# Kernel tuning notes

Measured on AMD Instinct MI355X. Metric: run time of the kernel, lower is better.

Reference implementation:

```python
import jax, jax.numpy as jnp
import numpy as np

N_NODES = 100000
N_EDGES = 3200000
NUM_GRAPHS = 128
IN_DIM = 15
HID = 64


def setup_inputs() -> dict:
    key = jax.random.key(0)
    ks = jax.random.split(key, 12)
    x = jax.random.normal(ks[0], (N_NODES, IN_DIM), dtype=jnp.float32)
    edge_index = jax.random.randint(ks[1], (2, N_EDGES), 0, N_NODES, dtype=jnp.int64)
    batch = jnp.sort(jax.random.randint(ks[2], (N_NODES,), 0, NUM_GRAPHS, dtype=jnp.int64))
    # Glorot-style weights for the 4 GCNConv layers, zero biases (PyG default)
    def glorot(k, fan_in, fan_out):
        s = jnp.sqrt(6.0 / (fan_in + fan_out))
        return jax.random.uniform(k, (fan_in, fan_out), jnp.float32, -s, s)
    return {
        "x": x,
        "w1": glorot(ks[3], IN_DIM, HID), "b1": jnp.zeros((HID,), jnp.float32),
        "w2": glorot(ks[4], HID, HID),    "b2": jnp.zeros((HID,), jnp.float32),
        "w3": glorot(ks[5], HID, HID),    "b3": jnp.zeros((HID,), jnp.float32),
        "w4": glorot(ks[6], HID, HID),    "b4": jnp.zeros((HID,), jnp.float32),
        "edge_index": edge_index,
        "batch": batch,
    }


def _gcn_norm(edge_index, num_nodes):
    # PyG gcn_norm with add_self_loops=True: A_hat = A + I, norm = d^-1/2[src] * d^-1/2[dst]
    loops = jnp.arange(num_nodes, dtype=edge_index.dtype)
    src = jnp.concatenate([edge_index[0], loops])
    dst = jnp.concatenate([edge_index[1], loops])
    deg = jax.ops.segment_sum(jnp.ones_like(dst, dtype=jnp.float32), dst,
                              num_segments=num_nodes)
    dis = jnp.where(deg > 0, jax.lax.rsqrt(deg), 0.0)
    norm = dis[src] * dis[dst]  # [E + N]
    return src, dst, norm


def _gcn_conv(h, w, b, src, dst, norm, num_nodes):
    h = h @ w                               # linear transform first (PyG order)
    msg = h[src] * norm[:, None]            # gather + scale  [E+N, HID]
    agg = jax.ops.segment_sum(msg, dst, num_segments=num_nodes)  # scatter-add
    return agg + b


def reference(x, w1, b1, w2, b2, w3, b3, w4, b4, edge_index, batch):
    n = x.shape[0]
    src, dst, norm = _gcn_norm(edge_index, n)
    h = jax.nn.relu(_gcn_conv(x, w1, b1, src, dst, norm, n))
    h = jax.nn.relu(_gcn_conv(h, w2, b2, src, dst, norm, n))
    h = jax.nn.relu(_gcn_conv(h, w3, b3, src, dst, norm, n))
    h = jax.nn.relu(_gcn_conv(h, w4, b4, src, dst, norm, n))
    # global_mean_pool over graph ids
    sums = jax.ops.segment_sum(h, batch, num_segments=NUM_GRAPHS)
    cnts = jax.ops.segment_sum(jnp.ones((n,), jnp.float32), batch,
                               num_segments=NUM_GRAPHS)
    return sums / jnp.maximum(cnts, 1.0)[:, None]
```

## Files before the change

kernel.cpp:

```cpp
#include <hip/hip_runtime.h>
#include <hip/hip_fp16.h>

#define NN 100000
#define NE 3200000
#define NG 128
#define HID 64

#define BSH 9
#define BNODES 512
#define NBK ((NN + BNODES - 1) / BNODES)
#define CCH 4096

typedef __attribute__((ext_vector_type(2))) _Float16 half2v;
typedef __attribute__((ext_vector_type(4))) _Float16 half4v;

#if __has_builtin(__builtin_amdgcn_fdot2)
#define FDOT2(v, o, a) __builtin_amdgcn_fdot2((v), (o), (a), false)
#else
static __device__ inline float FDOT2(half2v v, half2v o, float a) {
    return a + (float)v.x * (float)o.x + (float)v.y * (float)o.y;
}
#endif

__global__ __launch_bounds__(256) void bcount_kernel(const int* __restrict__ dst,
                                                     int* __restrict__ bcnt, int E) {
    __shared__ int h[NBK];
    for (int i = threadIdx.x; i < NBK; i += 256) h[i] = 0;
    __syncthreads();
    for (int e = blockIdx.x * 256 + threadIdx.x; e < E; e += gridDim.x * 256)
        atomicAdd(&h[dst[e] >> BSH], 1);
    __syncthreads();
    for (int i = threadIdx.x; i < NBK; i += 256)
        if (h[i]) atomicAdd(&bcnt[i], h[i]);
}

__global__ __launch_bounds__(256) void bscan_kernel(const int* __restrict__ bcnt,
                                                    int* __restrict__ bbase,
                                                    int* __restrict__ bcur, int E) {
    __shared__ int s[NBK];
    int t = threadIdx.x;
    if (t < NBK) s[t] = bcnt[t];
    __syncthreads();
    if (t == 0) {
        int acc = 0;
        for (int i = 0; i < NBK; ++i) { int v = s[i]; s[i] = acc; acc += v; }
    }
    __syncthreads();
    if (t < NBK) { bbase[t] = s[t]; bcur[t] = s[t]; }
    if (t == 0) bbase[NBK] = E;
}

__global__ __launch_bounds__(256) void bscatter_kernel(const int* __restrict__ src,
                                                       const int* __restrict__ dst,
                                                       int* __restrict__ bcur,
                                                       unsigned* __restrict__ pairs,
                                                       int E) {
    __shared__ unsigned stage[CCH];
    __shared__ unsigned char bb[CCH];
    __shared__ int cnt[NBK];
    __shared__ int base[NBK];
    const int e0 = blockIdx.x * CCH;
    const int n  = min(CCH, E - e0);
    if (n <= 0) return;
    for (int i = threadIdx.x; i < NBK; i += 256) cnt[i] = 0;
    __syncthreads();
    for (int i = threadIdx.x; i < n; i += 256) {
        int s = src[e0 + i], d = dst[e0 + i];
        int b = d >> BSH;
        stage[i] = ((unsigned)(d & (BNODES - 1)) << 17) | (unsigned)s;
        bb[i] = (unsigned char)b;
        atomicAdd(&cnt[b], 1);
    }
    __syncthreads();
    for (int i = threadIdx.x; i < NBK; i += 256) {
        int c = cnt[i];
        base[i] = c ? atomicAdd(&bcur[i], c) : 0;
        cnt[i] = 0;
    }
    __syncthreads();
    for (int i = threadIdx.x; i < n; i += 256) {
        int b = bb[i];
        int pos = base[b] + atomicAdd(&cnt[b], 1);
        pairs[pos] = stage[i];
    }
}

__global__ __launch_bounds__(256) void csr_kernel(const unsigned* __restrict__ pairs,
                                                  const int* __restrict__ bbase,
                                                  int* __restrict__ rowptr,
                                                  int* __restrict__ csr_src,
                                                  float* __restrict__ dis,
                                                  int N, int E) {
    __shared__ int hist[BNODES];
    __shared__ int cur[BNODES];
    __shared__ int s[256];
    const int b     = blockIdx.x;
    const int t     = threadIdx.x;
    const int node0 = b << BSH;
    const int nn    = min(BNODES, N - node0);
    const int p0 = bbase[b], p1 = bbase[b + 1];

    for (int i = t; i < BNODES; i += 256) hist[i] = 0;
    __syncthreads();
    for (int i = p0 + t; i < p1; i += 256)
        atomicAdd(&hist[pairs[i] >> 17], 1);
    __syncthreads();

    int h0 = hist[2 * t], h1 = hist[2 * t + 1];
    int v = h0 + h1;
    s[t] = v;
    __syncthreads();
    for (int off = 1; off < 256; off <<= 1) {
        int u = (t >= off) ? s[t - off] : 0;
        __syncthreads();
        s[t] += u;
        __syncthreads();
    }
    int excl = s[t] - v;
    int e0 = p0 + excl;
    int e1 = e0 + h0;
    if (2 * t < nn) {
        rowptr[node0 + 2 * t] = e0;
        dis[node0 + 2 * t] = rsqrtf((float)h0 + 1.0f);
        cur[2 * t] = e0;
    }
    if (2 * t + 1 < nn) {
        rowptr[node0 + 2 * t + 1] = e1;
        dis[node0 + 2 * t + 1] = rsqrtf((float)h1 + 1.0f);
        cur[2 * t + 1] = e1;
    }
    if (b == NBK - 1 && t == 0) rowptr[N] = E;
    __syncthreads();

    for (int i = p0 + t; i < p1; i += 256) {
        unsigned p = pairs[i];
        int pos = atomicAdd(&cur[p >> 17], 1);
        csr_src[pos] = (int)(p & 0x1FFFFu);
    }
}

__global__ __launch_bounds__(256) void xprep_kernel(const float* __restrict__ x,
                                                    const float* __restrict__ dis,
                                                    __half* __restrict__ x16h, int N) {
    int gid = blockIdx.x * 256 + threadIdx.x;
    if (gid >= N * 16) return;
    int node = gid >> 4, k = gid & 15;
    float v = (k < 15) ? x[node * 15 + k] * dis[node] : 0.0f;
    x16h[gid] = __float2half(v);
}

__global__ __launch_bounds__(256) void gather16_kernel(const half4v* __restrict__ xh,
                                                       const int* __restrict__ csr_src,
                                                       const int* __restrict__ rowptr,
                                                       const float* __restrict__ dis,
                                                       float4* __restrict__ aggx, int N) {
    const int gid  = blockIdx.x * 256 + threadIdx.x;
    const int node = gid >> 2;
    if (node >= N) return;
    const int l  = threadIdx.x & 3;
    const int gb = threadIdx.x & 60;
    const int start = rowptr[node], end = rowptr[node + 1];
    const half2v ONEX = {(_Float16)1.0f, (_Float16)0.0f};
    const half2v ONEY = {(_Float16)0.0f, (_Float16)1.0f};
    float a0 = 0.0f, a1 = 0.0f, a2 = 0.0f, a3 = 0.0f;
    for (int j0 = start; j0 < end; j0 += 4) {
        int j   = j0 + l;
        int s   = (j < end) ? csr_src[j] : 0;
        int cnt = min(4, end - j0);
#pragma unroll
        for (int k = 0; k < 4; ++k) {
            int sk = __shfl(s, gb + k);
            if (k < cnt) {
                half4v v = xh[sk * 4 + l];
                half2v p0 = __builtin_shufflevector(v, v, 0, 1);
                half2v p1 = __builtin_shufflevector(v, v, 2, 3);
                a0 = FDOT2(p0, ONEX, a0);
                a1 = FDOT2(p0, ONEY, a1);
                a2 = FDOT2(p1, ONEX, a2);
                a3 = FDOT2(p1, ONEY, a3);
            }
        }
    }
    half4v sv = xh[node * 4 + l];
    half2v s0 = __builtin_shufflevector(sv, sv, 0, 1);
    half2v s1 = __builtin_shufflevector(sv, sv, 2, 3);
    a0 += (float)s0.x; a1 += (float)s0.y;
    a2 += (float)s1.x; a3 += (float)s1.y;
    float sn = dis[node];
    aggx[(size_t)node * 4 + l] = make_float4(sn * a0, sn * a1, sn * a2, sn * a3);
}

__global__ __launch_bounds__(256) void gemm12_kernel(const float* __restrict__ in,
                                                     const float* __restrict__ w1,
                                                     const float* __restrict__ b1,
                                                     const float* __restrict__ w2,
                                                     const float* __restrict__ dis,
                                                     __half* __restrict__ th_out, int N) {
    __shared__ float w1_s[16 * 64];
    __shared__ float in_s[64 * 17];
    __shared__ float w2_s[64 * 64];
    __shared__ float h_s[64 * 65];
    const int tid  = threadIdx.x;
    const int row0 = blockIdx.x * 64;
    const int rows = min(64, N - row0);

    for (int i = tid; i < 16 * 64; i += 256) w1_s[i] = (i < 15 * 64) ? w1[i] : 0.0f;
    for (int i = tid; i < 64 * 64; i += 256) w2_s[i] = w2[i];
    for (int i = tid; i < rows * 16; i += 256) {
        int r = i >> 4, k = i & 15;
        in_s[r * 17 + k] = in[(size_t)(row0 + r) * 16 + k];
    }
    __syncthreads();

    const int r  = tid & 63;
    const int cg = tid >> 6;
    {
        float acc[16];
#pragma unroll
        for (int i = 0; i < 16; ++i) acc[i] = 0.0f;
#pragma unroll
        for (int k = 0; k < 16; ++k) {
            float a = in_s[r * 17 + k];
#pragma unroll
            for (int cc = 0; cc < 16; ++cc)
                acc[cc] += a * w1_s[k * 64 + cg * 16 + cc];
        }
#pragma unroll
        for (int cc = 0; cc < 16; ++cc)
            h_s[r * 65 + cg * 16 + cc] = fmaxf(acc[cc] + b1[cg * 16 + cc], 0.0f);
    }
    __syncthreads();
    {
        const float2* w2v = reinterpret_cast<const float2*>(w2_s);
        float2 acc2[8];
#pragma unroll
        for (int i = 0; i < 8; ++i) acc2[i] = make_float2(0.0f, 0.0f);
#pragma unroll
        for (int k = 0; k < 64; ++k) {
            float a = h_s[r * 65 + k];
            const float2* wk = w2v + k * 32 + cg * 8;
#pragma unroll
            for (int i = 0; i < 8; ++i) {
                float2 wv = wk[i];
                acc2[i].x += a * wv.x;
                acc2[i].y += a * wv.y;
            }
        }
        const int row = row0 + r;
        if (row < N) {
            float sd = dis[row];
            __align__(16) __half2 hh[8];
#pragma unroll
            for (int i = 0; i < 8; ++i)
                hh[i] = __floats2half2_rn(acc2[i].x * sd, acc2[i].y * sd);
            float4* tp = reinterpret_cast<float4*>(th_out + (size_t)row * HID + cg * 16);
            tp[0] = reinterpret_cast<float4*>(hh)[0];
            tp[1] = reinterpret_cast<float4*>(hh)[1];
        }
    }
}

__global__ __launch_bounds__(256) void fusedGG_kernel(const half2v* __restrict__ th_in,
                                                      const int* __restrict__ csr_src,
                                                      const int* __restrict__ rowptr,
                                                      const float* __restrict__ dis,
                                                      const float* __restrict__ w,
                                                      const float* __restrict__ bias,
                                                      __half* __restrict__ th_out, int N) {
    __shared__ float w_s[64 * 64];
    __shared__ float r_s[8][64];
    const int tid = threadIdx.x;
    {
        const float4* wsrc = reinterpret_cast<const float4*>(w);
        float4* wdst = reinterpret_cast<float4*>(w_s);
        for (int i = tid; i < 1024; i += 256) wdst[i] = wsrc[i];
    }
    const int g    = tid >> 5;
    const int node = blockIdx.x * 8 + g;
    const int l    = tid & 31;
    const int hb   = tid & 32;
    float u0 = 0.0f, u1 = 0.0f;
    if (node < N) {
        const int start = rowptr[node], end = rowptr[node + 1];
        const half2v* tl = th_in + l;
        const half2v ONEX = {(_Float16)1.0f, (_Float16)0.0f};
        const half2v ONEY = {(_Float16)0.0f, (_Float16)1.0f};
        float ax = 0.0f, ay = 0.0f;
        for (int j0 = start; j0 < end; j0 += 32) {
            int j   = j0 + l;
            int s   = (j < end) ? csr_src[j] : 0;
            int cnt = min(32, end - j0);
            int k = 0;
            for (; k + 16 <= cnt; k += 16) {
                int sk[16];
#pragma unroll
                for (int u = 0; u < 16; ++u) sk[u] = __shfl(s, hb + k + u);
                half2v v[16];
#pragma unroll
                for (int u = 0; u < 16; ++u) v[u] = tl[sk[u] * 32];
#pragma unroll
                for (int u = 0; u < 16; ++u) {
                    ax = FDOT2(v[u], ONEX, ax);
                    ay = FDOT2(v[u], ONEY, ay);
                }
            }
            for (; k + 4 <= cnt; k += 4) {
                int s0 = __shfl(s, hb + k);
                int s1 = __shfl(s, hb + k + 1);
                int s2 = __shfl(s, hb + k + 2);
                int s3 = __shfl(s, hb + k + 3);
                half2v v0 = tl[s0 * 32];
                half2v v1 = tl[s1 * 32];
                half2v v2 = tl[s2 * 32];
                half2v v3 = tl[s3 * 32];
                ax = FDOT2(v0, ONEX, ax); ay = FDOT2(v0, ONEY, ay);
                ax = FDOT2(v1, ONEX, ax); ay = FDOT2(v1, ONEY, ay);
                ax = FDOT2(v2, ONEX, ax); ay = FDOT2(v2, ONEY, ay);
                ax = FDOT2(v3, ONEX, ax); ay = FDOT2(v3, ONEY, ay);
            }
            for (; k < cnt; ++k) {
                half2v v = tl[__shfl(s, hb + k) * 32];
                ax += (float)v.x; ay += (float)v.y;
            }
        }
        half2v self = tl[node * 32];
        ax += (float)self.x; ay += (float)self.y;
        float sn = dis[node];
        float2 bv = reinterpret_cast<const float2*>(bias)[l];
        u0 = fmaxf(sn * ax + bv.x, 0.0f);
        u1 = fmaxf(sn * ay + bv.y, 0.0f);
    }
    reinterpret_cast<float2*>(r_s[g])[l] = make_float2(u0, u1);
    __syncthreads();
    if (node < N) {
        const float2* wv = reinterpret_cast<const float2*>(w_s);
        float c0 = 0.0f, c1 = 0.0f;
#pragma unroll 8
        for (int k = 0; k < 64; ++k) {
            float u = r_s[g][k];
            float2 ww = wv[k * 32 + l];
            c0 += u * ww.x;
            c1 += u * ww.y;
        }
        float sd = dis[node];
        reinterpret_cast<__half2*>(th_out)[(size_t)node * 32 + l] =
            __floats2half2_rn(c0 * sd, c1 * sd);
    }
}

__global__ __launch_bounds__(256) void gatherh_kernel(const half2v* __restrict__ th,
                                                      const int* __restrict__ csr_src,
                                                      const int* __restrict__ rowptr,
                                                      const float* __restrict__ dis,
                                                      float* __restrict__ agg, int N) {
    const int gid  = blockIdx.x * 256 + threadIdx.x;
    const int node = gid >> 5;
    if (node >= N) return;
    const int l  = threadIdx.x & 31;
    const int hb = threadIdx.x & 32;
    const int start = rowptr[node], end = rowptr[node + 1];
    const half2v* tl = th + l;
    const half2v ONEX = {(_Float16)1.0f, (_Float16)0.0f};
    const half2v ONEY = {(_Float16)0.0f, (_Float16)1.0f};
    float ax = 0.0f, ay = 0.0f;
    for (int j0 = start; j0 < end; j0 += 32) {
        int j   = j0 + l;
        int s   = (j < end) ? csr_src[j] : 0;
        int cnt = min(32, end - j0);
        int k = 0;
        for (; k + 16 <= cnt; k += 16) {
            int sk[16];
#pragma unroll
            for (int u = 0; u < 16; ++u) sk[u] = __shfl(s, hb + k + u);
            half2v v[16];
#pragma unroll
            for (int u = 0; u < 16; ++u) v[u] = tl[sk[u] * 32];
#pragma unroll
            for (int u = 0; u < 16; ++u) {
                ax = FDOT2(v[u], ONEX, ax);
                ay = FDOT2(v[u], ONEY, ay);
            }
        }
        for (; k + 4 <= cnt; k += 4) {
            int s0 = __shfl(s, hb + k);
            int s1 = __shfl(s, hb + k + 1);
            int s2 = __shfl(s, hb + k + 2);
            int s3 = __shfl(s, hb + k + 3);
            half2v v0 = tl[s0 * 32];
            half2v v1 = tl[s1 * 32];
            half2v v2 = tl[s2 * 32];
            half2v v3 = tl[s3 * 32];
            ax = FDOT2(v0, ONEX, ax); ay = FDOT2(v0, ONEY, ay);
            ax = FDOT2(v1, ONEX, ax); ay = FDOT2(v1, ONEY, ay);
            ax = FDOT2(v2, ONEX, ax); ay = FDOT2(v2, ONEY, ay);
            ax = FDOT2(v3, ONEX, ax); ay = FDOT2(v3, ONEY, ay);
        }
        for (; k < cnt; ++k) {
            half2v v = tl[__shfl(s, hb + k) * 32];
            ax += (float)v.x; ay += (float)v.y;
        }
    }
    half2v self = tl[node * 32];
    ax += (float)self.x; ay += (float)self.y;
    float sn = dis[node];
    reinterpret_cast<float2*>(agg)[(size_t)node * 32 + l] =
        make_float2(sn * ax, sn * ay);
}

__global__ __launch_bounds__(256) void pool_kernel(const float* __restrict__ agg,
                                                   const float* __restrict__ b4,
                                                   const int* __restrict__ batch,
                                                   float* __restrict__ sums,
                                                   float* __restrict__ cnts, int N) {
    __shared__ float lsum[NG * HID];
    __shared__ float lcnt[NG];
    const int tid  = threadIdx.x;
    const int base = blockIdx.x * 256;
    const int last = min(base + 256, N) - 1;
    const int gfirst = batch[base];
    const int glast  = batch[last];
    const int span   = glast - gfirst + 1;

    for (int i = tid; i < span * HID; i += 256) lsum[i] = 0.0f;
    for (int i = tid; i < span; i += 256) lcnt[i] = 0.0f;
    __syncthreads();

    const int f = tid & 63, sub = tid >> 6;
    for (int n = base + sub; n < min(base + 256, N); n += 4) {
        int g = batch[n];
        float v = fmaxf(agg[(size_t)n * HID + f] + b4[f], 0.0f);
        atomicAdd(&lsum[(g - gfirst) * HID + f], v);
        if (f == 0) atomicAdd(&lcnt[g - gfirst], 1.0f);
    }
    __syncthreads();

    for (int i = tid; i < span * HID; i += 256)
        atomicAdd(&sums[(size_t)gfirst * HID + i], lsum[i]);
    for (int i = tid; i < span; i += 256) atomicAdd(&cnts[gfirst + i], lcnt[i]);
}

__global__ __launch_bounds__(256) void finalize_kernel(const float* __restrict__ sums,
                                                       const float* __restrict__ cnts,
                                                       float* __restrict__ out) {
    int i = blockIdx.x * 256 + threadIdx.x;
    if (i < NG * HID) out[i] = sums[i] / fmaxf(cnts[i >> 6], 1.0f);
}

extern "C" void kernel_launch(void* const* d_in, const int* in_sizes, int n_in,
                              void* d_out, int out_size, void* d_ws, size_t ws_size,
                              hipStream_t stream) {
    const float* x  = (const float*)d_in[0];
    const float* w1 = (const float*)d_in[1];
    const float* b1 = (const float*)d_in[2];
    const float* w2 = (const float*)d_in[3];
    const float* b2 = (const float*)d_in[4];
    const float* w3 = (const float*)d_in[5];
    const float* b3 = (const float*)d_in[6];
    const float* w4 = (const float*)d_in[7];
    const float* b4 = (const float*)d_in[8];
    const int* ei    = (const int*)d_in[9];
    const int* batch = (const int*)d_in[10];
    const int* src = ei;
    const int* dst = ei + NE;

    float*    AGG     = (float*)d_ws;
    __half*   thB     = (__half*)d_ws;
    __half*   thA     = (__half*)(AGG + (size_t)NN * HID);
    unsigned* pairs   = (unsigned*)(thA + (size_t)NN * HID);
    __half*   x16h    = (__half*)pairs;
    float*    aggx    = (float*)(x16h + (size_t)NN * 16);
    int*      csr_src = (int*)((char*)pairs + (size_t)NE * 4);
    int*      rowptr  = csr_src + NE;
    float*    dis     = (float*)(rowptr + NN + 1);
    int*      bcnt    = (int*)(dis + NN);
    int*      bbase   = bcnt + NBK;
    int*      bcur    = bbase + NBK + 1;
    float*    sums    = (float*)(bcur + NBK);
    float*    cnts    = sums + NG * HID;

    float* out = (float*)d_out;

    const int NB  = (NN + 255) / 256;
    const int GB  = (NN + 63) / 64;
    const int XB  = (NN * 16 + 255) / 256;
    const int OB  = (NN * 4 + 255) / 256;
    const int HB  = (NN * 32 + 255) / 256;
    const int FB  = (NN + 7) / 8;
    const int CB  = (NE + CCH - 1) / CCH;

    hipMemsetAsync(bcnt, 0, NBK * sizeof(int), stream);
    hipMemsetAsync(sums, 0, (NG * HID + NG) * sizeof(float), stream);

    bcount_kernel<<<512, 256, 0, stream>>>(dst, bcnt, NE);
    bscan_kernel<<<1, 256, 0, stream>>>(bcnt, bbase, bcur, NE);
    bscatter_kernel<<<CB, 256, 0, stream>>>(src, dst, bcur, pairs, NE);
    csr_kernel<<<NBK, 256, 0, stream>>>(pairs, bbase, rowptr, csr_src, dis, NN, NE);

    xprep_kernel<<<XB, 256, 0, stream>>>(x, dis, x16h, NN);
    gather16_kernel<<<OB, 256, 0, stream>>>((const half4v*)x16h, csr_src, rowptr, dis,
                                            (float4*)aggx, NN);
    gemm12_kernel<<<GB, 256, 0, stream>>>(aggx, w1, b1, w2, dis, thA, NN);
    fusedGG_kernel<<<FB, 256, 0, stream>>>((const half2v*)thA, csr_src, rowptr, dis,
                                           w3, b2, thB, NN);
    fusedGG_kernel<<<FB, 256, 0, stream>>>((const half2v*)thB, csr_src, rowptr, dis,
                                           w4, b3, thA, NN);
    gatherh_kernel<<<HB, 256, 0, stream>>>((const half2v*)thA, csr_src, rowptr, dis, AGG, NN);

    pool_kernel<<<NB, 256, 0, stream>>>(AGG, b4, batch, sums, cnts, NN);
    finalize_kernel<<<(NG * HID + 255) / 256, 256, 0, stream>>>(sums, cnts, out);
}
```

Before: 531.9 us.

## Gather half-precision rows with 8 lanes per node using 16-byte loads

The aggregation kernels now give each node 8 lanes instead of 32, and each lane loads a 16-byte half8 chunk of a neighbour's row rather than 4 bytes. Neighbour indices are prefetched one chunk ahead. In the fused kernel the 64x64 transform now exchanges activations by wave shuffles instead of shared memory. The aim is fewer, wider memory transactions and more nodes per wave to hide gather latency, at the cost of more registers per lane and a shuffle-heavy matmul.

After: 553.5 us. +4.1%, slower.

```diff
diff --git a/kernel.cpp b/kernel.cpp
--- a/kernel.cpp
+++ b/kernel.cpp
@@ -13,6 +13,7 @@
 
 typedef __attribute__((ext_vector_type(2))) _Float16 half2v;
 typedef __attribute__((ext_vector_type(4))) _Float16 half4v;
+typedef __attribute__((ext_vector_type(8))) _Float16 half8v;
 
 #if __has_builtin(__builtin_amdgcn_fdot2)
 #define FDOT2(v, o, a) __builtin_amdgcn_fdot2((v), (o), (a), false)
@@ -21,6 +22,17 @@
     return a + (float)v.x * (float)o.x + (float)v.y * (float)o.y;
 }
 #endif
+
+#define ACC8(vv) do {                                                   \
+    half2v p0 = __builtin_shufflevector(vv, vv, 0, 1);                  \
+    half2v p1 = __builtin_shufflevector(vv, vv, 2, 3);                  \
+    half2v p2 = __builtin_shufflevector(vv, vv, 4, 5);                  \
+    half2v p3 = __builtin_shufflevector(vv, vv, 6, 7);                  \
+    a[0] = FDOT2(p0, ONEX, a[0]); a[1] = FDOT2(p0, ONEY, a[1]);         \
+    a[2] = FDOT2(p1, ONEX, a[2]); a[3] = FDOT2(p1, ONEY, a[3]);         \
+    a[4] = FDOT2(p2, ONEX, a[4]); a[5] = FDOT2(p2, ONEY, a[5]);         \
+    a[6] = FDOT2(p3, ONEX, a[6]); a[7] = FDOT2(p3, ONEY, a[7]);         \
+} while (0)
 
 __global__ __launch_bounds__(256) void bcount_kernel(const int* __restrict__ dst,
                                                      int* __restrict__ bcnt, int E) {
@@ -260,7 +272,42 @@
     }
 }
 
-__global__ __launch_bounds__(256) void fusedGG_kernel(const half2v* __restrict__ th_in,
+__device__ __forceinline__ void gather8(const half8v* __restrict__ tl,
+                                        const int* __restrict__ csr_src,
+                                        int start, int end, int node,
+                                        int q, int gb, float a[8]) {
+    const half2v ONEX = {(_Float16)1.0f, (_Float16)0.0f};
+    const half2v ONEY = {(_Float16)0.0f, (_Float16)1.0f};
+    int j0 = start;
+    int s  = (start + q < end) ? csr_src[start + q] : 0;
+    while (j0 < end) {
+        const int cnt = end - j0;
+        const int jn  = j0 + 8;
+        int spre = (jn + q < end) ? csr_src[jn + q] : 0;
+        if (cnt >= 8) {
+            int sk[8];
+#pragma unroll
+            for (int u = 0; u < 8; ++u) sk[u] = __shfl(s, gb + u);
+            half8v v[8];
+#pragma unroll
+            for (int u = 0; u < 8; ++u) v[u] = tl[sk[u] * 8];
+#pragma unroll
+            for (int u = 0; u < 8; ++u) { half8v vv = v[u]; ACC8(vv); }
+        } else {
+            for (int k = 0; k < cnt; ++k) {
+                int sk = __shfl(s, gb + k);
+                half8v vv = tl[sk * 8];
+                ACC8(vv);
+            }
+        }
+        s = spre;
+        j0 = jn;
+    }
+    half8v sv = tl[node * 8];
+    ACC8(sv);
+}
+
+__global__ __launch_bounds__(256) void fusedGG_kernel(const __half* __restrict__ th_in,
                                                       const int* __restrict__ csr_src,
                                                       const int* __restrict__ rowptr,
                                                       const float* __restrict__ dis,
@@ -268,143 +315,88 @@
                                                       const float* __restrict__ bias,
                                                       __half* __restrict__ th_out, int N) {
     __shared__ float w_s[64 * 64];
-    __shared__ float r_s[8][64];
     const int tid = threadIdx.x;
     {
         const float4* wsrc = reinterpret_cast<const float4*>(w);
         float4* wdst = reinterpret_cast<float4*>(w_s);
         for (int i = tid; i < 1024; i += 256) wdst[i] = wsrc[i];
     }
-    const int g    = tid >> 5;
-    const int node = blockIdx.x * 8 + g;
-    const int l    = tid & 31;
-    const int hb   = tid & 32;
-    float u0 = 0.0f, u1 = 0.0f;
+    const int g    = tid >> 3;
+    const int q    = tid & 7;
+    const int gb   = tid & 56;
+    const int node = blockIdx.x * 32 + g;
+
+    float uv[8];
+#pragma unroll
+    for (int i = 0; i < 8; ++i) uv[i] = 0.0f;
+
     if (node < N) {
-        const int start = rowptr[node], end = rowptr[node + 1];
-        const half2v* tl = th_in + l;
-        const half2v ONEX = {(_Float16)1.0f, (_Float16)0.0f};
-        const half2v ONEY = {(_Float16)0.0f, (_Float16)1.0f};
-        float ax = 0.0f, ay = 0.0f;
-        for (int j0 = start; j0 < end; j0 += 32) {
-            int j   = j0 + l;
-            int s   = (j < end) ? csr_src[j] : 0;
-            int cnt = min(32, end - j0);
-            int k = 0;
-            for (; k + 16 <= cnt; k += 16) {
-                int sk[16];
-#pragma unroll
-                for (int u = 0; u < 16; ++u) sk[u] = __shfl(s, hb + k + u);
-                half2v v[16];
-#pragma unroll
-                for (int u = 0; u < 16; ++u) v[u] = tl[sk[u] * 32];
-#pragma unroll
-                for (int u = 0; u < 16; ++u) {
-                    ax = FDOT2(v[u], ONEX, ax);
-                    ay = FDOT2(v[u], ONEY, ay);
-                }
-            }
-            for (; k + 4 <= cnt; k += 4) {
-                int s0 = __shfl(s, hb + k);
-                int s1 = __shfl(s, hb + k + 1);
-                int s2 = __shfl(s, hb + k + 2);
-                int s3 = __shfl(s, hb + k + 3);
-                half2v v0 = tl[s0 * 32];
-                half2v v1 = tl[s1 * 32];
-                half2v v2 = tl[s2 * 32];
-                half2v v3 = tl[s3 * 32];
-                ax = FDOT2(v0, ONEX, ax); ay = FDOT2(v0, ONEY, ay);
-                ax = FDOT2(v1, ONEX, ax); ay = FDOT2(v1, ONEY, ay);
-                ax = FDOT2(v2, ONEX, ax); ay = FDOT2(v2, ONEY, ay);
-                ax = FDOT2(v3, ONEX, ax); ay = FDOT2(v3, ONEY, ay);
-            }
-            for (; k < cnt; ++k) {
-                half2v v = tl[__shfl(s, hb + k) * 32];
-                ax += (float)v.x; ay += (float)v.y;
-            }
+        float a[8];
+#pragma unroll
+        for (int i = 0; i < 8; ++i) a[i] = 0.0f;
+        const half8v* tl = reinterpret_cast<const half8v*>(th_in) + q;
+        gather8(tl, csr_src, rowptr[node], rowptr[node + 1], node, q, gb, a);
+        const float sn = dis[node];
+        const float4* bp = reinterpret_cast<const float4*>(bias);
+        const float4 b0 = bp[q * 2], b1 = bp[q * 2 + 1];
+        uv[0] = fmaxf(fmaf(sn, a[0], b0.x), 0.0f);
+        uv[1] = fmaxf(fmaf(sn, a[1], b0.y), 0.0f);
+        uv[2] = fmaxf(fmaf(sn, a[2], b0.z), 0.0f);
+        uv[3] = fmaxf(fmaf(sn, a[3], b0.w), 0.0f);
+        uv[4] = fmaxf(fmaf(sn, a[4], b1.x), 0.0f);
+        uv[5] = fmaxf(fmaf(sn, a[5], b1.y), 0.0f);
+        uv[6] = fmaxf(fmaf(sn, a[6], b1.z), 0.0f);
+        uv[7] = fmaxf(fmaf(sn, a[7], b1.w), 0.0f);
+    }
+    __syncthreads();
+
+    float c[8];
+#pragma unroll
+    for (int i = 0; i < 8; ++i) c[i] = 0.0f;
+    const float4* wv4 = reinterpret_cast<const float4*>(w_s);
+#pragma unroll
+    for (int k0 = 0; k0 < 64; k0 += 8) {
+        const int owner = gb + (k0 >> 3);
+#pragma unroll
+        for (int u = 0; u < 8; ++u) {
+            float uk = __shfl(uv[u], owner);
+            float4 w0 = wv4[((k0 + u) << 4) + (q << 1)];
+            float4 w1 = wv4[((k0 + u) << 4) + (q << 1) + 1];
+            c[0] += uk * w0.x; c[1] += uk * w0.y; c[2] += uk * w0.z; c[3] += uk * w0.w;
+            c[4] += uk * w1.x; c[5] += uk * w1.y; c[6] += uk * w1.z; c[7] += uk * w1.w;
         }
-        half2v self = tl[node * 32];
-        ax += (float)self.x; ay += (float)self.y;
-        float sn = dis[node];
-        float2 bv = reinterpret_cast<const float2*>(bias)[l];
-        u0 = fmaxf(sn * ax + bv.x, 0.0f);
-        u1 = fmaxf(sn * ay + bv.y, 0.0f);
-    }
-    reinterpret_cast<float2*>(r_s[g])[l] = make_float2(u0, u1);
-    __syncthreads();
+    }
     if (node < N) {
-        const float2* wv = reinterpret_cast<const float2*>(w_s);
-        float c0 = 0.0f, c1 = 0.0f;
-#pragma unroll 8
-        for (int k = 0; k < 64; ++k) {
-            float u = r_s[g][k];
-            float2 ww = wv[k * 32 + l];
-            c0 += u * ww.x;
-            c1 += u * ww.y;
-        }
-        float sd = dis[node];
-        reinterpret_cast<__half2*>(th_out)[(size_t)node * 32 + l] =
-            __floats2half2_rn(c0 * sd, c1 * sd);
-    }
-}
-
-__global__ __launch_bounds__(256) void gatherh_kernel(const half2v* __restrict__ th,
+        const float sd = dis[node];
+        __align__(16) __half2 hh[4];
+#pragma unroll
+        for (int i = 0; i < 4; ++i)
+            hh[i] = __floats2half2_rn(c[2 * i] * sd, c[2 * i + 1] * sd);
+        reinterpret_cast<float4*>(th_out)[node * 8 + q] =
+            *reinterpret_cast<const float4*>(hh);
+    }
+}
+
+__global__ __launch_bounds__(256) void gatherh_kernel(const __half* __restrict__ th,
                                                       const int* __restrict__ csr_src,
                                                       const int* __restrict__ rowptr,
                                                       const float* __restrict__ dis,
                                                       float* __restrict__ agg, int N) {
-    const int gid  = blockIdx.x * 256 + threadIdx.x;
-    const int node = gid >> 5;
+    const int tid  = threadIdx.x;
+    const int g    = tid >> 3;
+    const int q    = tid & 7;
+    const int gb   = tid & 56;
+    const int node = blockIdx.x * 32 + g;
     if (node >= N) return;
-    const int l  = threadIdx.x & 31;
-    const int hb = threadIdx.x & 32;
-    const int start = rowptr[node], end = rowptr[node + 1];
-    const half2v* tl = th + l;
-    const half2v ONEX = {(_Float16)1.0f, (_Float16)0.0f};
-    const half2v ONEY = {(_Float16)0.0f, (_Float16)1.0f};
-    float ax = 0.0f, ay = 0.0f;
-    for (int j0 = start; j0 < end; j0 += 32) {
-        int j   = j0 + l;
-        int s   = (j < end) ? csr_src[j] : 0;
-        int cnt = min(32, end - j0);
-        int k = 0;
-        for (; k + 16 <= cnt; k += 16) {
-            int sk[16];
-#pragma unroll
-            for (int u = 0; u < 16; ++u) sk[u] = __shfl(s, hb + k + u);
-            half2v v[16];
-#pragma unroll
-            for (int u = 0; u < 16; ++u) v[u] = tl[sk[u] * 32];
-#pragma unroll
-            for (int u = 0; u < 16; ++u) {
-                ax = FDOT2(v[u], ONEX, ax);
-                ay = FDOT2(v[u], ONEY, ay);
-            }
-        }
-        for (; k + 4 <= cnt; k += 4) {
-            int s0 = __shfl(s, hb + k);
-            int s1 = __shfl(s, hb + k + 1);
-            int s2 = __shfl(s, hb + k + 2);
-            int s3 = __shfl(s, hb + k + 3);
-            half2v v0 = tl[s0 * 32];
-            half2v v1 = tl[s1 * 32];
-            half2v v2 = tl[s2 * 32];
-            half2v v3 = tl[s3 * 32];
-            ax = FDOT2(v0, ONEX, ax); ay = FDOT2(v0, ONEY, ay);
-            ax = FDOT2(v1, ONEX, ax); ay = FDOT2(v1, ONEY, ay);
-            ax = FDOT2(v2, ONEX, ax); ay = FDOT2(v2, ONEY, ay);
-            ax = FDOT2(v3, ONEX, ax); ay = FDOT2(v3, ONEY, ay);
-        }
-        for (; k < cnt; ++k) {
-            half2v v = tl[__shfl(s, hb + k) * 32];
-            ax += (float)v.x; ay += (float)v.y;
-        }
-    }
-    half2v self = tl[node * 32];
-    ax += (float)self.x; ay += (float)self.y;
-    float sn = dis[node];
-    reinterpret_cast<float2*>(agg)[(size_t)node * 32 + l] =
-        make_float2(sn * ax, sn * ay);
+    float a[8];
+#pragma unroll
+    for (int i = 0; i < 8; ++i) a[i] = 0.0f;
+    const half8v* tl = reinterpret_cast<const half8v*>(th) + q;
+    gather8(tl, csr_src, rowptr[node], rowptr[node + 1], node, q, gb, a);
+    const float sn = dis[node];
+    float4* ap = reinterpret_cast<float4*>(agg) + node * 16 + q * 2;
+    ap[0] = make_float4(sn * a[0], sn * a[1], sn * a[2], sn * a[3]);
+    ap[1] = make_float4(sn * a[4], sn * a[5], sn * a[6], sn * a[7]);
 }
 
 __global__ __launch_bounds__(256) void pool_kernel(const float* __restrict__ agg,
@@ -484,8 +476,7 @@
     const int GB  = (NN + 63) / 64;
     const int XB  = (NN * 16 + 255) / 256;
     const int OB  = (NN * 4 + 255) / 256;
-    const int HB  = (NN * 32 + 255) / 256;
-    const int FB  = (NN + 7) / 8;
+    const int FB  = (NN + 31) / 32;
     const int CB  = (NE + CCH - 1) / CCH;
 
     hipMemsetAsync(bcnt, 0, NBK * sizeof(int), stream);
@@ -500,11 +491,9 @@
     gather16_kernel<<<OB, 256, 0, stream>>>((const half4v*)x16h, csr_src, rowptr, dis,
                                             (float4*)aggx, NN);
     gemm12_kernel<<<GB, 256, 0, stream>>>(aggx, w1, b1, w2, dis, thA, NN);
-    fusedGG_kernel<<<FB, 256, 0, stream>>>((const half2v*)thA, csr_src, rowptr, dis,
-                                           w3, b2, thB, NN);
-    fusedGG_kernel<<<FB, 256, 0, stream>>>((const half2v*)thB, csr_src, rowptr, dis,
-                                           w4, b3, thA, NN);
-    gatherh_kernel<<<HB, 256, 0, stream>>>((const half2v*)thA, csr_src, rowptr, dis, AGG, NN);
+    fusedGG_kernel<<<FB, 256, 0, stream>>>(thA, csr_src, rowptr, dis, w3, b2, thB, NN);
+    fusedGG_kernel<<<FB, 256, 0, stream>>>(thB, csr_src, rowptr, dis, w4, b3, thA, NN);
+    gatherh_kernel<<<FB, 256, 0, stream>>>(thA, csr_src, rowptr, dis, AGG, NN);
 
     pool_kernel<<<NB, 256, 0, stream>>>(AGG, b4, batch, sums, cnts, NN);
     finalize_kernel<<<(NG * HID + 255) / 256, 256, 0, stream>>>(sums, cnts, out);
```
